# Kernel tuning notes

Measured on AMD Instinct MI355X. Metric: run time of the kernel, lower is better.

## Reference

```python
import jax, jax.numpy as jnp
import numpy as np


def setup_inputs() -> dict:
    key = jax.random.key(0)
    k1, k2 = jax.random.split(key)
    B, N, C, S = 4, 16384, 128, 32
    # normalized point coordinates in [-1, 1]
    ptcloud = jax.random.uniform(k1, (B, N, 3), jnp.float32, -1.0, 1.0)
    cubic_features = jax.random.normal(k2, (B, C, S, S, S), jnp.float32)
    return {"ptcloud": ptcloud, "cubic_features": cubic_features, "neighborhood_size": 1}


def reference(ptcloud, cubic_features, neighborhood_size):
    # ptcloud: [B, N, 3] in [-1, 1]; cubic_features: [B, C, S, S, S]
    B, C, S = cubic_features.shape[0], cubic_features.shape[1], cubic_features.shape[2]
    N = ptcloud.shape[1]
    h = S / 2.0
    pt = ptcloud * h + h  # scaled to [0, S]
    ns = neighborhood_size - 1
    lower = jnp.floor(pt).astype(jnp.int32)  # [B, N, 3]
    # CUDA kernel: upper = ceil(pt); if lower == upper: upper += 1 -> upper == lower + 1 always;
    # vertices range over [lower - ns, upper + ns] => 2*neighborhood_size values per axis
    offs = jnp.arange(-ns, ns + 2, dtype=jnp.int32)  # K = 2*neighborhood_size
    idx3 = lower[:, :, None, :] + offs[None, None, :, None]  # [B, N, K, 3]
    ii, jj, kk = idx3[..., 0], idx3[..., 1], idx3[..., 2]
    # cartesian product of per-axis candidates -> [B, N, K, K, K]
    I = ii[:, :, :, None, None]
    J = jj[:, :, None, :, None]
    Kz = kk[:, :, None, None, :]
    valid = (I >= 0) & (I < S) & (J >= 0) & (J < S) & (Kz >= 0) & (Kz < S)
    flat = (jnp.clip(I, 0, S - 1) * S + jnp.clip(J, 0, S - 1)) * S + jnp.clip(Kz, 0, S - 1)
    K = offs.shape[0]
    V = K * K * K  # vertices per point
    flat = flat.reshape(B, N, V)
    valid = valid.reshape(B, N, V)
    cf = cubic_features.reshape(B, C, S * S * S)
    gathered = jax.vmap(lambda f, i: f[:, i])(cf, flat)  # [B, C, N, V]
    point_features = jnp.transpose(gathered, (0, 2, 3, 1)) * valid[..., None].astype(cubic_features.dtype)
    return point_features  # [B, N, V, C]
```

## Files before the change

### kernel.cpp

```cpp
#include <hip/hip_runtime.h>
#include <hip/hip_bf16.h>

#define PB 4
#define PN 16384
#define PC 128
#define PS 32
#define PS3 (PS * PS * PS)
#define PV 8
#define PTS_PER_BLK 4

typedef float f32x4 __attribute__((ext_vector_type(4)));
typedef uint  u32x2 __attribute__((ext_vector_type(2)));

__device__ __forceinline__ ushort f32_to_bf16_rne(float f) {
    uint32_t u = __float_as_uint(f);
    u += 0x7FFFu + ((u >> 16) & 1u);
    return (ushort)(u >> 16);
}

__global__ __launch_bounds__(256) void cfs_transpose_bf16_kernel(
        const float* __restrict__ in, ushort* __restrict__ cft) {
    __shared__ uint tile[32][66];
    const int b   = blockIdx.y;
    const int s0  = blockIdx.x * 32;
    const int tid = threadIdx.x;

    const float* src = in + (size_t)b * PC * PS3 + s0;
    const int s4 = (tid & 7) * 4;
    const int cp = tid >> 3;

    #pragma unroll
    for (int it = 0; it < 2; ++it) {
        const int cw = cp + it * 32;
        const int c  = cw * 2;
        f32x4 a = __builtin_nontemporal_load(
            reinterpret_cast<const f32x4*>(src + (size_t)c * PS3 + s4));
        f32x4 d = __builtin_nontemporal_load(
            reinterpret_cast<const f32x4*>(src + (size_t)(c + 1) * PS3 + s4));
        tile[s4 + 0][cw] = (uint)f32_to_bf16_rne(a.x) | ((uint)f32_to_bf16_rne(d.x) << 16);
        tile[s4 + 1][cw] = (uint)f32_to_bf16_rne(a.y) | ((uint)f32_to_bf16_rne(d.y) << 16);
        tile[s4 + 2][cw] = (uint)f32_to_bf16_rne(a.z) | ((uint)f32_to_bf16_rne(d.z) << 16);
        tile[s4 + 3][cw] = (uint)f32_to_bf16_rne(a.w) | ((uint)f32_to_bf16_rne(d.w) << 16);
    }
    __syncthreads();

    const int cl = tid & 31;
    const int sr = tid >> 5;
    #pragma unroll
    for (int it = 0; it < 4; ++it) {
        const int s = sr + it * 8;
        u32x2 w = *reinterpret_cast<const u32x2*>(&tile[s][cl * 2]);
        *reinterpret_cast<u32x2*>(cft + ((size_t)b * PS3 + s0 + s) * PC + cl * 4) = w;
    }
}

__device__ __forceinline__ void cfs_point_corner(const float* __restrict__ pt,
                                                 int bn, int v,
                                                 bool& ok, int& flat) {
    const float px = pt[(size_t)bn * 3 + 0];
    const float py = pt[(size_t)bn * 3 + 1];
    const float pz = pt[(size_t)bn * 3 + 2];
    const int ix0 = (int)floorf(__fadd_rn(__fmul_rn(px, 16.0f), 16.0f));
    const int iy0 = (int)floorf(__fadd_rn(__fmul_rn(py, 16.0f), 16.0f));
    const int iz0 = (int)floorf(__fadd_rn(__fmul_rn(pz, 16.0f), 16.0f));
    const int ii = ix0 + ((v >> 2) & 1);
    const int jj = iy0 + ((v >> 1) & 1);
    const int kk = iz0 + (v & 1);
    ok = ((unsigned)ii < (unsigned)PS) &
         ((unsigned)jj < (unsigned)PS) &
         ((unsigned)kk < (unsigned)PS);
    const int ci = min(max(ii, 0), PS - 1);
    const int cj = min(max(jj, 0), PS - 1);
    const int ck = min(max(kk, 0), PS - 1);
    flat = (ci * PS + cj) * PS + ck;
}

__global__ __launch_bounds__(256) void cfs_gather_bf16_kernel(
        const float* __restrict__ pt, const ushort* __restrict__ cft,
        float* __restrict__ out) {
    const int t   = threadIdx.x;
    const int v   = t >> 5;
    const int cl  = t & 31;
    const int bn0 = blockIdx.x * PTS_PER_BLK;
    const int b   = bn0 >> 14;

    #pragma unroll
    for (int h = 0; h < PTS_PER_BLK; ++h) {
        const int bn = bn0 + h;
        bool ok; int flat;
        cfs_point_corner(pt, bn, v, ok, flat);
        const float m = ok ? 1.0f : 0.0f;

        const u32x2* row = reinterpret_cast<const u32x2*>(
            cft + ((size_t)b * PS3 + flat) * PC);
        u32x2 w = row[cl];
        f32x4 r;
        r.x = __uint_as_float(w.x << 16) * m;
        r.y = __uint_as_float(w.x & 0xffff0000u) * m;
        r.z = __uint_as_float(w.y << 16) * m;
        r.w = __uint_as_float(w.y & 0xffff0000u) * m;
        __builtin_nontemporal_store(
            r, reinterpret_cast<f32x4*>(out) + (size_t)bn * 256 + t);
    }
}

__global__ void cfs_gather_d_kernel(const float* __restrict__ pt,
                                    const float* __restrict__ cf,
                                    float* __restrict__ out) {
    const int bn = blockIdx.x;
    const int b  = bn >> 14;
    const int t  = threadIdx.x;
    const int v  = t >> 5;
    const int c4 = (t & 31) << 2;

    bool ok; int flat;
    cfs_point_corner(pt, bn, v, ok, flat);

    f32x4 r = (f32x4)(0.f);
    if (ok) {
        const float* basep = cf + (size_t)b * PC * PS3 + flat;
        r.x = basep[(size_t)(c4 + 0) * PS3];
        r.y = basep[(size_t)(c4 + 1) * PS3];
        r.z = basep[(size_t)(c4 + 2) * PS3];
        r.w = basep[(size_t)(c4 + 3) * PS3];
    }
    *(reinterpret_cast<f32x4*>(out) + (size_t)bn * 256 + t) = r;
}

extern "C" void kernel_launch(void* const* d_in, const int* in_sizes, int n_in,
                              void* d_out, int out_size, void* d_ws, size_t ws_size,
                              hipStream_t stream) {
    const float* pt = (const float*)d_in[0];
    const float* cf = (const float*)d_in[1];
    float* out = (float*)d_out;

    const size_t needed = (size_t)PB * PS3 * PC * sizeof(ushort);
    if (d_ws != nullptr && ws_size >= needed) {
        ushort* cft = (ushort*)d_ws;
        cfs_transpose_bf16_kernel<<<dim3(PS3 / 32, PB), dim3(256), 0, stream>>>(cf, cft);
        cfs_gather_bf16_kernel<<<dim3(PB * PN / PTS_PER_BLK), dim3(256), 0, stream>>>(
            pt, cft, out);
    } else {
        cfs_gather_d_kernel<<<dim3(PB * PN), dim3(256), 0, stream>>>(pt, cf, out);
    }
}
```

Before: 78.38 us.

## Enlarge transpose tiles with XOR swizzle and batch gather loads per block

```diff
diff --git a/kernel.cpp b/kernel.cpp
--- a/kernel.cpp
+++ b/kernel.cpp
@@ -7,50 +7,56 @@
 #define PS 32
 #define PS3 (PS * PS * PS)
 #define PV 8
-#define PTS_PER_BLK 4
+#define GPTS 8
 
 typedef float f32x4 __attribute__((ext_vector_type(4)));
 typedef uint  u32x2 __attribute__((ext_vector_type(2)));
 
-__device__ __forceinline__ ushort f32_to_bf16_rne(float f) {
-    uint32_t u = __float_as_uint(f);
-    u += 0x7FFFu + ((u >> 16) & 1u);
-    return (ushort)(u >> 16);
+__device__ __forceinline__ uint bf16pack(float lo, float hi) {
+    uint ul = __float_as_uint(lo);
+    ul += 0x7FFFu + ((ul >> 16) & 1u);
+    uint uh = __float_as_uint(hi);
+    uh += 0x7FFFu + ((uh >> 16) & 1u);
+    return (ul >> 16) | (uh & 0xFFFF0000u);
 }
 
 __global__ __launch_bounds__(256) void cfs_transpose_bf16_kernel(
         const float* __restrict__ in, ushort* __restrict__ cft) {
-    __shared__ uint tile[32][66];
-    const int b   = blockIdx.y;
-    const int s0  = blockIdx.x * 32;
-    const int tid = threadIdx.x;
+    __shared__ uint tile[256][64];
+    const int b  = blockIdx.y;
+    const int s0 = blockIdx.x * 256;
+    const int t  = threadIdx.x;
+    const int l  = t & 63;
+    const int wv = t >> 6;
+    const int s4 = l * 4;
+    const int xv = (l & 15) << 1;
 
-    const float* src = in + (size_t)b * PC * PS3 + s0;
-    const int s4 = (tid & 7) * 4;
-    const int cp = tid >> 3;
-
-    #pragma unroll
-    for (int it = 0; it < 2; ++it) {
-        const int cw = cp + it * 32;
-        const int c  = cw * 2;
+    const float* src = in + (size_t)b * PC * PS3 + s0 + s4;
+    #pragma unroll 4
+    for (int it = 0; it < 16; ++it) {
+        const int cp = wv * 16 + it;
+        const int c  = cp * 2;
         f32x4 a = __builtin_nontemporal_load(
-            reinterpret_cast<const f32x4*>(src + (size_t)c * PS3 + s4));
+            reinterpret_cast<const f32x4*>(src + (size_t)c * PS3));
         f32x4 d = __builtin_nontemporal_load(
-            reinterpret_cast<const f32x4*>(src + (size_t)(c + 1) * PS3 + s4));
-        tile[s4 + 0][cw] = (uint)f32_to_bf16_rne(a.x) | ((uint)f32_to_bf16_rne(d.x) << 16);
-        tile[s4 + 1][cw] = (uint)f32_to_bf16_rne(a.y) | ((uint)f32_to_bf16_rne(d.y) << 16);
-        tile[s4 + 2][cw] = (uint)f32_to_bf16_rne(a.z) | ((uint)f32_to_bf16_rne(d.z) << 16);
-        tile[s4 + 3][cw] = (uint)f32_to_bf16_rne(a.w) | ((uint)f32_to_bf16_rne(d.w) << 16);
+            reinterpret_cast<const f32x4*>(src + (size_t)(c + 1) * PS3));
+        const int col = cp ^ xv;
+        tile[s4 + 0][col] = bf16pack(a.x, d.x);
+        tile[s4 + 1][col] = bf16pack(a.y, d.y);
+        tile[s4 + 2][col] = bf16pack(a.z, d.z);
+        tile[s4 + 3][col] = bf16pack(a.w, d.w);
     }
     __syncthreads();
 
-    const int cl = tid & 31;
-    const int sr = tid >> 5;
-    #pragma unroll
-    for (int it = 0; it < 4; ++it) {
-        const int s = sr + it * 8;
-        u32x2 w = *reinterpret_cast<const u32x2*>(&tile[s][cl * 2]);
-        *reinterpret_cast<u32x2*>(cft + ((size_t)b * PS3 + s0 + s) * PC + cl * 4) = w;
+    const int cl = l & 31;
+    const int r0 = (l >> 5) + wv * 2;
+    ushort* dst = cft + ((size_t)b * PS3 + s0) * PC;
+    #pragma unroll 8
+    for (int it = 0; it < 32; ++it) {
+        const int r   = it * 8 + r0;
+        const int col = (cl * 2) ^ (((r >> 2) & 15) << 1);
+        u32x2 w = *reinterpret_cast<const u32x2*>(&tile[r][col]);
+        *reinterpret_cast<u32x2*>(dst + (size_t)r * PC + cl * 4) = w;
     }
 }
 
@@ -81,26 +87,33 @@
     const int t   = threadIdx.x;
     const int v   = t >> 5;
     const int cl  = t & 31;
-    const int bn0 = blockIdx.x * PTS_PER_BLK;
+    const int bn0 = blockIdx.x * GPTS;
     const int b   = bn0 >> 14;
+    const ushort* cfb = cft + (size_t)b * PS3 * PC;
+
+    int   flat[GPTS];
+    float m[GPTS];
+    #pragma unroll
+    for (int h = 0; h < GPTS; ++h) {
+        bool ok;
+        cfs_point_corner(pt, bn0 + h, v, ok, flat[h]);
+        m[h] = ok ? 1.0f : 0.0f;
+    }
+
+    u32x2 w[GPTS];
+    #pragma unroll
+    for (int h = 0; h < GPTS; ++h)
+        w[h] = reinterpret_cast<const u32x2*>(cfb + (size_t)flat[h] * PC)[cl];
 
     #pragma unroll
-    for (int h = 0; h < PTS_PER_BLK; ++h) {
-        const int bn = bn0 + h;
-        bool ok; int flat;
-        cfs_point_corner(pt, bn, v, ok, flat);
-        const float m = ok ? 1.0f : 0.0f;
-
-        const u32x2* row = reinterpret_cast<const u32x2*>(
-            cft + ((size_t)b * PS3 + flat) * PC);
-        u32x2 w = row[cl];
+    for (int h = 0; h < GPTS; ++h) {
         f32x4 r;
-        r.x = __uint_as_float(w.x << 16) * m;
-        r.y = __uint_as_float(w.x & 0xffff0000u) * m;
-        r.z = __uint_as_float(w.y << 16) * m;
-        r.w = __uint_as_float(w.y & 0xffff0000u) * m;
+        r.x = __uint_as_float(w[h].x << 16)          * m[h];
+        r.y = __uint_as_float(w[h].x & 0xffff0000u)  * m[h];
+        r.z = __uint_as_float(w[h].y << 16)          * m[h];
+        r.w = __uint_as_float(w[h].y & 0xffff0000u)  * m[h];
         __builtin_nontemporal_store(
-            r, reinterpret_cast<f32x4*>(out) + (size_t)bn * 256 + t);
+            r, reinterpret_cast<f32x4*>(out) + (size_t)(bn0 + h) * 256 + t);
     }
 }
 
@@ -137,8 +150,8 @@
     const size_t needed = (size_t)PB * PS3 * PC * sizeof(ushort);
     if (d_ws != nullptr && ws_size >= needed) {
         ushort* cft = (ushort*)d_ws;
-        cfs_transpose_bf16_kernel<<<dim3(PS3 / 32, PB), dim3(256), 0, stream>>>(cf, cft);
-        cfs_gather_bf16_kernel<<<dim3(PB * PN / PTS_PER_BLK), dim3(256), 0, stream>>>(
+        cfs_transpose_bf16_kernel<<<dim3(PS3 / 256, PB), dim3(256), 0, stream>>>(cf, cft);
+        cfs_gather_bf16_kernel<<<dim3(PB * PN / GPTS), dim3(256), 0, stream>>>(
             pt, cft, out);
     } else {
         cfs_gather_d_kernel<<<dim3(PB * PN), dim3(256), 0, stream>>>(pt, cf, out);
```

After: 82.17 us. +4.8%, slower.
